# Performance work log

Measured on AMD Instinct MI355X. Metric: run time of the kernel, lower is better.

## Reference

```python
import jax, jax.numpy as jnp
import numpy as np

B, S, D = 4, 2048, 768
H = 12
HD = D // H  # 64


def setup_inputs() -> dict:
    key = jax.random.key(0)
    ks = jax.random.split(key, 7)
    scale = 1.0 / np.sqrt(D)
    return {
        "hidden_states": jax.random.normal(ks[0], (B, S, D), dtype=jnp.float32),
        "Wq": jax.random.normal(ks[1], (D, D), dtype=jnp.float32) * scale,
        "bq": jnp.zeros((D,), dtype=jnp.float32),
        "Wk": jax.random.normal(ks[2], (D, D), dtype=jnp.float32) * scale,
        "bk": jnp.zeros((D,), dtype=jnp.float32),
        "Wv": jax.random.normal(ks[3], (D, D), dtype=jnp.float32) * scale,
        "bv": jnp.zeros((D,), dtype=jnp.float32),
    }


def _split_heads(x):
    # [B, S, D] -> [B, H, S, HD]
    b, s, _ = x.shape
    return x.reshape(b, s, H, HD).transpose(0, 2, 1, 3)


def reference(hidden_states, Wq, bq, Wk, bk, Wv, bv):
    q = _split_heads(hidden_states @ Wq + bq)
    k = _split_heads(hidden_states @ Wk + bk)
    v = _split_heads(hidden_states @ Wv + bv)
    # [B, H, S, S] attention scores (naive full materialization, as in source)
    scores = jnp.einsum("bhqd,bhkd->bhqk", q, k) / jnp.sqrt(jnp.float32(HD))
    attn = jax.nn.softmax(scores, axis=-1)  # dropout = identity (eval)
    ctx = jnp.einsum("bhqk,bhkd->bhqd", attn, v)
    # [B, H, S, HD] -> [B, S, D]
    return ctx.transpose(0, 2, 1, 3).reshape(hidden_states.shape[0], -1, H * HD)
```

## Files before the change

### kernel.cpp

```cpp
#include <hip/hip_runtime.h>
#include <cmath>

#define B_  4
#define S_  2048
#define D_  768
#define H_  12
#define HD_ 64
#define BH_ 48
#define N3_ 2304
#define M_  8192

typedef _Float16 half8  __attribute__((ext_vector_type(8)));
typedef _Float16 half4v __attribute__((ext_vector_type(4)));
typedef __fp16   fp16x2 __attribute__((ext_vector_type(2)));
typedef __fp16   fp16x4 __attribute__((ext_vector_type(4)));
typedef float    floatx4 __attribute__((ext_vector_type(4)));

typedef const unsigned int __attribute__((address_space(1)))* gas_u32;
typedef unsigned int __attribute__((address_space(3)))* las_u32;

#define LOG2E 1.4426950408889634f
#define NEG_C (-5.0f * 1.4426950408889634f)

__global__ void cvt_f32_f16(const float* __restrict__ src,
                            _Float16* __restrict__ dst, int n) {
  int i = (blockIdx.x * blockDim.x + threadIdx.x) * 4;
  if (i < n) {
    float4 v = *(const float4*)(src + i);
    half4v h = {(_Float16)v.x, (_Float16)v.y, (_Float16)v.z, (_Float16)v.w};
    *(half4v*)(dst + i) = h;
  }
}

__global__ __launch_bounds__(256) void transpose_cvt_w(
    const float* __restrict__ W, _Float16* __restrict__ Wt) {
  __shared__ float tile[32][33];
  const int k0 = blockIdx.x * 32, n0 = blockIdx.y * 32;
  const int r = threadIdx.x >> 3, c4 = (threadIdx.x & 7) * 4;
  float4 v = *(const float4*)(W + (size_t)(k0 + r) * D_ + n0 + c4);
  tile[r][c4 + 0] = v.x; tile[r][c4 + 1] = v.y;
  tile[r][c4 + 2] = v.z; tile[r][c4 + 3] = v.w;
  __syncthreads();
  half4v h = {(_Float16)tile[c4 + 0][r], (_Float16)tile[c4 + 1][r],
              (_Float16)tile[c4 + 2][r], (_Float16)tile[c4 + 3][r]};
  *(half4v*)(Wt + (size_t)(n0 + r) * D_ + k0 + c4) = h;
}

__global__ __launch_bounds__(256, 3) void gemm_qkv(
    const _Float16* __restrict__ Xh, const _Float16* __restrict__ Wt3,
    const float* __restrict__ bq, const float* __restrict__ bk,
    const float* __restrict__ bv,
    _Float16* __restrict__ qo, _Float16* __restrict__ ko,
    _Float16* __restrict__ vto) {
  __shared__ __align__(16) char gsm[36864];
  _Float16* As = (_Float16*)gsm;
  _Float16* Bs = (_Float16*)(gsm + 16384);
  const int tid = threadIdx.x;
  const int w = tid >> 6, lane = tid & 63;
  const int tx = lane & 15, quad = lane >> 4;
  const int nBase = blockIdx.x * 128;
  const int mBase = blockIdx.y * 128;
  const int wm = (w & 1) * 64, wn = (w >> 1) * 64;

  floatx4 acc[4][4];
  #pragma unroll
  for (int i = 0; i < 4; ++i)
    #pragma unroll
    for (int j = 0; j < 4; ++j) acc[i][j] = (floatx4){0.f, 0.f, 0.f, 0.f};

  const int ldRow = lane >> 3;
  const int ldCol = (lane & 7) * 8;

  for (int k0 = 0; k0 < D_; k0 += 64) {
    __syncthreads();
    #pragma unroll
    for (int io = 0; io < 4; ++io) {
      int row = w * 32 + io * 8;
      const _Float16* ga =
          Xh + (size_t)(mBase + row + ldRow) * D_ + k0 + ldCol;
      __builtin_amdgcn_global_load_lds((gas_u32)(const void*)ga,
                                       (las_u32)(void*)&As[row * 64], 16, 0, 0);
      const _Float16* gb =
          Wt3 + (size_t)(nBase + row + ldRow) * D_ + k0 + ldCol;
      __builtin_amdgcn_global_load_lds((gas_u32)(const void*)gb,
                                       (las_u32)(void*)&Bs[row * 64], 16, 0, 0);
    }
    __syncthreads();

    half8 af0[4], af1[4], bf0[4], bf1[4];
    #pragma unroll
    for (int i = 0; i < 4; ++i) {
      af0[i] = *(const half8*)&As[(wm + 16 * i + tx) * 64 + quad * 8];
      af1[i] = *(const half8*)&As[(wm + 16 * i + tx) * 64 + quad * 8 + 32];
    }
    #pragma unroll
    for (int j = 0; j < 4; ++j) {
      bf0[j] = *(const half8*)&Bs[(wn + 16 * j + tx) * 64 + quad * 8];
      bf1[j] = *(const half8*)&Bs[(wn + 16 * j + tx) * 64 + quad * 8 + 32];
    }
    #pragma unroll
    for (int i = 0; i < 4; ++i)
      #pragma unroll
      for (int j = 0; j < 4; ++j) {
        acc[i][j] = __builtin_amdgcn_mfma_f32_16x16x32_f16(af0[i], bf0[j], acc[i][j], 0, 0, 0);
        acc[i][j] = __builtin_amdgcn_mfma_f32_16x16x32_f16(af1[i], bf1[j], acc[i][j], 0, 0, 0);
      }
  }

  const int region = nBase / 768;
  const int b = mBase >> 11;
  const int sBase = mBase & (S_ - 1);

  if (region < 2) {
    const float scale = (region == 0) ? 0.125f * LOG2E : 1.0f;
    const float* bias = (region == 0) ? bq : bk;
    _Float16* dst = (region == 0) ? qo : ko;
    const int nLoc = (nBase % 768) + wn;
    #pragma unroll
    for (int j = 0; j < 4; ++j) {
      int n = nLoc + 16 * j + tx;
      int h = n >> 6, d = n & 63;
      float bb = bias[n];
      #pragma unroll
      for (int i = 0; i < 4; ++i)
        #pragma unroll
        for (int r = 0; r < 4; ++r) {
          int m = mBase + wm + 16 * i + quad * 4 + r;
          int s = m & (S_ - 1);
          dst[((size_t)(b * H_ + h) * S_ + s) * HD_ + d] =
              (_Float16)((acc[i][j][r] + bb) * scale);
        }
    }
  } else {
    __syncthreads();
    _Float16 (*Ct)[144] = (_Float16(*)[144])gsm;
    const int nV = nBase - 1536;
    #pragma unroll
    for (int j = 0; j < 4; ++j) {
      int nl = wn + 16 * j + tx;
      float bb = bv[nV + nl];
      #pragma unroll
      for (int i = 0; i < 4; ++i)
        #pragma unroll
        for (int r = 0; r < 4; ++r)
          Ct[nl][wm + 16 * i + quad * 4 + r] = (_Float16)(acc[i][j][r] + bb);
    }
    __syncthreads();
    #pragma unroll
    for (int io = 0; io < 8; ++io) {
      int idx = io * 256 + tid;
      int nl = idx >> 4;
      int sc = (idx & 15) * 8;
      int n = nV + nl, h = n >> 6, d = n & 63;
      half8 hv = *(const half8*)&Ct[nl][sc];
      *(half8*)(vto + (((size_t)(b * H_ + h) * HD_) + d) * S_ + sBase + sc) = hv;
    }
  }
}

__global__ __launch_bounds__(512, 4) void attn_mfma(
    const _Float16* __restrict__ qh, const _Float16* __restrict__ kh,
    const _Float16* __restrict__ vth, float* __restrict__ out) {
  __shared__ __align__(16) char smem[36864];
  _Float16 (*Ks2)[64][72]  = (_Float16(*)[64][72])smem;
  _Float16 (*Vts2)[64][72] = (_Float16(*)[64][72])(smem + 18432);
  float (*Of)[68] = (float(*)[68])smem;
  float* lbuf = (float*)(smem + 34816);

  const int tid = threadIdx.x;
  const int bh = blockIdx.y;
  const int qBase = blockIdx.x * 128;
  const int w = tid >> 6, lane = tid & 63;
  const int half = w >> 2, wq = w & 3;
  const int tx = lane & 15, quad = lane >> 4;

  const _Float16* kp = kh + (size_t)bh * S_ * HD_;
  const _Float16* vtp = vth + (size_t)bh * HD_ * S_;

  half8 bq[2][2];
  #pragma unroll
  for (int g = 0; g < 2; ++g) {
    const _Float16* qp =
        qh + ((size_t)bh * S_ + qBase + wq * 32 + g * 16 + tx) * HD_;
    bq[g][0] = *(const half8*)(qp + quad * 8);
    bq[g][1] = *(const half8*)(qp + quad * 8 + 32);
  }

  floatx4 o_acc[2][4];
  #pragma unroll
  for (int g = 0; g < 2; ++g)
    #pragma unroll
    for (int j = 0; j < 4; ++j) o_acc[g][j] = (floatx4){0.f, 0.f, 0.f, 0.f};
  float l_loc[2] = {0.f, 0.f};

  const int th = tid & 255;
  const int kr = th >> 3, kc = (th & 7) * 8;

  for (int it = 0; it < S_ / 128; ++it) {
    const int kt0 = it * 128 + half * 64;
    __syncthreads();
    #pragma unroll
    for (int io = 0; io < 2; ++io) {
      int row = kr + io * 32;
      *(half8*)&Ks2[half][row][kc] =
          *(const half8*)(kp + (size_t)(kt0 + row) * HD_ + kc);
      *(half8*)&Vts2[half][row][kc] =
          *(const half8*)(vtp + (size_t)row * S_ + kt0 + kc);
    }
    __syncthreads();

    #pragma unroll
    for (int t = 0; t < 4; ++t) {
      half8 ka0 = *(const half8*)&Ks2[half][16 * t + tx][quad * 8];
      half8 ka1 = *(const half8*)&Ks2[half][16 * t + tx][quad * 8 + 32];
      fp16x4 pf[2];
      #pragma unroll
      for (int g = 0; g < 2; ++g) {
        __builtin_amdgcn_s_setprio(1);
        floatx4 st = __builtin_amdgcn_mfma_f32_16x16x32_f16(
            ka0, bq[g][0], (floatx4){NEG_C, NEG_C, NEG_C, NEG_C}, 0, 0, 0);
        st = __builtin_amdgcn_mfma_f32_16x16x32_f16(ka1, bq[g][1], st, 0, 0, 0);
        __builtin_amdgcn_s_setprio(0);
        float p0 = __builtin_amdgcn_exp2f(st[0]);
        float p1 = __builtin_amdgcn_exp2f(st[1]);
        float p2 = __builtin_amdgcn_exp2f(st[2]);
        float p3 = __builtin_amdgcn_exp2f(st[3]);
        l_loc[g] += (p0 + p1) + (p2 + p3);
        fp16x2 lo = __builtin_amdgcn_cvt_pkrtz(p0, p1);
        fp16x2 hi = __builtin_amdgcn_cvt_pkrtz(p2, p3);
        pf[g] = (fp16x4){lo.x, lo.y, hi.x, hi.y};
      }
      __builtin_amdgcn_s_setprio(1);
      #pragma unroll
      for (int j = 0; j < 4; ++j) {
        fp16x4 vb = *(const fp16x4*)&Vts2[half][16 * j + tx][16 * t + quad * 4];
        o_acc[0][j] = __builtin_amdgcn_mfma_f32_16x16x16f16(pf[0], vb, o_acc[0][j], 0, 0, 0);
        o_acc[1][j] = __builtin_amdgcn_mfma_f32_16x16x16f16(pf[1], vb, o_acc[1][j], 0, 0, 0);
      }
      __builtin_amdgcn_s_setprio(0);
    }
  }

  float lg[2];
  #pragma unroll
  for (int g = 0; g < 2; ++g) {
    lg[g] = l_loc[g];
    lg[g] += __shfl_xor(lg[g], 16, 64);
    lg[g] += __shfl_xor(lg[g], 32, 64);
  }

  __syncthreads();
  if (half == 1) {
    #pragma unroll
    for (int g = 0; g < 2; ++g) {
      int rowB = wq * 32 + g * 16;
      #pragma unroll
      for (int j = 0; j < 4; ++j)
        #pragma unroll
        for (int r = 0; r < 4; ++r)
          Of[rowB + quad * 4 + r][16 * j + tx] = o_acc[g][j][r];
      if (quad == 0) lbuf[rowB + tx] = lg[g];
    }
  }
  __syncthreads();
  if (half == 0) {
    const int b = bh / H_;
    const int h = bh % H_;
    #pragma unroll
    for (int g = 0; g < 2; ++g) {
      int rowB = wq * 32 + g * 16;
      float ltot = lg[g] + lbuf[rowB + tx];
      #pragma unroll
      for (int r = 0; r < 4; ++r) {
        int m = quad * 4 + r;
        float inv = 1.f / __shfl(ltot, m, 64);
        int s = qBase + rowB + m;
        #pragma unroll
        for (int j = 0; j < 4; ++j) {
          float o = o_acc[g][j][r] + Of[rowB + m][16 * j + tx];
          out[((size_t)b * S_ + s) * D_ + h * HD_ + 16 * j + tx] = o * inv;
        }
      }
    }
  }
}

extern "C" void kernel_launch(void* const* d_in, const int* in_sizes, int n_in,
                              void* d_out, int out_size, void* d_ws, size_t ws_size,
                              hipStream_t stream) {
  const float* X  = (const float*)d_in[0];
  const float* Wq = (const float*)d_in[1];
  const float* bq = (const float*)d_in[2];
  const float* Wk = (const float*)d_in[3];
  const float* bk = (const float*)d_in[4];
  const float* Wv = (const float*)d_in[5];
  const float* bv = (const float*)d_in[6];
  float* out = (float*)d_out;

  const size_t nX = (size_t)M_ * D_;
  const size_t nW = (size_t)D_ * D_;
  const size_t nQ = (size_t)BH_ * S_ * HD_;

  _Float16* Xh  = (_Float16*)d_ws;
  _Float16* Wt3 = Xh + nX;
  _Float16* qhb = Wt3 + 3 * nW;
  _Float16* khb = qhb + nQ;
  _Float16* vtb = khb + nQ;

  cvt_f32_f16<<<(int)(nX / 4 / 256), 256, 0, stream>>>(X, Xh, (int)nX);

  dim3 gridT(D_ / 32, D_ / 32);
  transpose_cvt_w<<<gridT, 256, 0, stream>>>(Wq, Wt3);
  transpose_cvt_w<<<gridT, 256, 0, stream>>>(Wk, Wt3 + nW);
  transpose_cvt_w<<<gridT, 256, 0, stream>>>(Wv, Wt3 + 2 * nW);

  dim3 gridG(N3_ / 128, M_ / 128);
  gemm_qkv<<<gridG, 256, 0, stream>>>(Xh, Wt3, bq, bk, bv, qhb, khb, vtb);

  dim3 gridA(S_ / 128, BH_);
  attn_mfma<<<gridA, 512, 0, stream>>>(qhb, khb, vtb, out);
}
```

Baseline: 210.7 us.

## Use 16x16x32 MFMA for PV with permuted K rows and register-prefetched tiles

Computes two QK^T score tiles per step and feeds the exponentiated probabilities as half8 operands into the K=32 MFMA for the PV product. This halves the number of PV MFMA instructions and V LDS reads. K rows are stored in LDS under a permutation so the score layout lines up with the wider MFMA's k-index order. The next K/V tile is also prefetched into registers during compute, so global loads overlap with MFMA work. This costs more registers, which could hurt occupancy under the 512x4 launch bounds.

```diff
diff --git a/kernel.cpp b/kernel.cpp
--- a/kernel.cpp
+++ b/kernel.cpp
@@ -173,6 +173,7 @@
   const int w = tid >> 6, lane = tid & 63;
   const int half = w >> 2, wq = w & 3;
   const int tx = lane & 15, quad = lane >> 4;
+  const int rbase = 16 * (tx >> 3) + 4 * ((tx >> 2) & 1) + (tx & 3);
 
   const _Float16* kp = kh + (size_t)bh * S_ * HD_;
   const _Float16* vtp = vth + (size_t)bh * HD_ * S_;
@@ -196,46 +197,82 @@
   const int th = tid & 255;
   const int kr = th >> 3, kc = (th & 7) * 8;
 
-  for (int it = 0; it < S_ / 128; ++it) {
-    const int kt0 = it * 128 + half * 64;
-    __syncthreads();
+  const int NT = S_ / 128;
+  half8 kst[2], vst[2];
+  {
+    const int kt0 = half * 64;
     #pragma unroll
     for (int io = 0; io < 2; ++io) {
       int row = kr + io * 32;
-      *(half8*)&Ks2[half][row][kc] =
-          *(const half8*)(kp + (size_t)(kt0 + row) * HD_ + kc);
-      *(half8*)&Vts2[half][row][kc] =
-          *(const half8*)(vtp + (size_t)row * S_ + kt0 + kc);
-    }
-    __syncthreads();
-
-    #pragma unroll
-    for (int t = 0; t < 4; ++t) {
-      half8 ka0 = *(const half8*)&Ks2[half][16 * t + tx][quad * 8];
-      half8 ka1 = *(const half8*)&Ks2[half][16 * t + tx][quad * 8 + 32];
-      fp16x4 pf[2];
+      kst[io] = *(const half8*)(kp + (size_t)(kt0 + row) * HD_ + kc);
+      vst[io] = *(const half8*)(vtp + (size_t)row * S_ + kt0 + kc);
+    }
+  }
+
+  for (int it = 0; it < NT; ++it) {
+    __syncthreads();
+    #pragma unroll
+    for (int io = 0; io < 2; ++io) {
+      int row = kr + io * 32;
+      int srow = (row & 51) | ((row & 4) << 1) | ((row & 8) >> 1);
+      *(half8*)&Ks2[half][srow][kc] = kst[io];
+      *(half8*)&Vts2[half][row][kc] = vst[io];
+    }
+    if (it + 1 < NT) {
+      const int kt1 = (it + 1) * 128 + half * 64;
+      #pragma unroll
+      for (int io = 0; io < 2; ++io) {
+        int row = kr + io * 32;
+        kst[io] = *(const half8*)(kp + (size_t)(kt1 + row) * HD_ + kc);
+        vst[io] = *(const half8*)(vtp + (size_t)row * S_ + kt1 + kc);
+      }
+    }
+    __syncthreads();
+
+    #pragma unroll
+    for (int T = 0; T < 2; ++T) {
+      floatx4 st[2][2];
+      #pragma unroll
+      for (int u = 0; u < 2; ++u) {
+        int lrow = rbase + 32 * T + 8 * u;
+        half8 ka0 = *(const half8*)&Ks2[half][lrow][quad * 8];
+        half8 ka1 = *(const half8*)&Ks2[half][lrow][quad * 8 + 32];
+        __builtin_amdgcn_s_setprio(1);
+        #pragma unroll
+        for (int g = 0; g < 2; ++g) {
+          st[g][u] = __builtin_amdgcn_mfma_f32_16x16x32_f16(
+              ka0, bq[g][0], (floatx4){NEG_C, NEG_C, NEG_C, NEG_C}, 0, 0, 0);
+          st[g][u] = __builtin_amdgcn_mfma_f32_16x16x32_f16(
+              ka1, bq[g][1], st[g][u], 0, 0, 0);
+        }
+        __builtin_amdgcn_s_setprio(0);
+      }
+      half8 pf[2];
       #pragma unroll
       for (int g = 0; g < 2; ++g) {
-        __builtin_amdgcn_s_setprio(1);
-        floatx4 st = __builtin_amdgcn_mfma_f32_16x16x32_f16(
-            ka0, bq[g][0], (floatx4){NEG_C, NEG_C, NEG_C, NEG_C}, 0, 0, 0);
-        st = __builtin_amdgcn_mfma_f32_16x16x32_f16(ka1, bq[g][1], st, 0, 0, 0);
-        __builtin_amdgcn_s_setprio(0);
-        float p0 = __builtin_amdgcn_exp2f(st[0]);
-        float p1 = __builtin_amdgcn_exp2f(st[1]);
-        float p2 = __builtin_amdgcn_exp2f(st[2]);
-        float p3 = __builtin_amdgcn_exp2f(st[3]);
-        l_loc[g] += (p0 + p1) + (p2 + p3);
-        fp16x2 lo = __builtin_amdgcn_cvt_pkrtz(p0, p1);
-        fp16x2 hi = __builtin_amdgcn_cvt_pkrtz(p2, p3);
-        pf[g] = (fp16x4){lo.x, lo.y, hi.x, hi.y};
+        float p0 = __builtin_amdgcn_exp2f(st[g][0][0]);
+        float p1 = __builtin_amdgcn_exp2f(st[g][0][1]);
+        float p2 = __builtin_amdgcn_exp2f(st[g][0][2]);
+        float p3 = __builtin_amdgcn_exp2f(st[g][0][3]);
+        float p4 = __builtin_amdgcn_exp2f(st[g][1][0]);
+        float p5 = __builtin_amdgcn_exp2f(st[g][1][1]);
+        float p6 = __builtin_amdgcn_exp2f(st[g][1][2]);
+        float p7 = __builtin_amdgcn_exp2f(st[g][1][3]);
+        l_loc[g] += ((p0 + p1) + (p2 + p3)) + ((p4 + p5) + (p6 + p7));
+        fp16x2 q0 = __builtin_amdgcn_cvt_pkrtz(p0, p1);
+        fp16x2 q1 = __builtin_amdgcn_cvt_pkrtz(p2, p3);
+        fp16x2 q2 = __builtin_amdgcn_cvt_pkrtz(p4, p5);
+        fp16x2 q3 = __builtin_amdgcn_cvt_pkrtz(p6, p7);
+        pf[g] = (half8){(_Float16)q0.x, (_Float16)q0.y, (_Float16)q1.x,
+                        (_Float16)q1.y, (_Float16)q2.x, (_Float16)q2.y,
+                        (_Float16)q3.x, (_Float16)q3.y};
       }
       __builtin_amdgcn_s_setprio(1);
       #pragma unroll
       for (int j = 0; j < 4; ++j) {
-        fp16x4 vb = *(const fp16x4*)&Vts2[half][16 * j + tx][16 * t + quad * 4];
-        o_acc[0][j] = __builtin_amdgcn_mfma_f32_16x16x16f16(pf[0], vb, o_acc[0][j], 0, 0, 0);
-        o_acc[1][j] = __builtin_amdgcn_mfma_f32_16x16x16f16(pf[1], vb, o_acc[1][j], 0, 0, 0);
+        half8 vb = *(const half8*)&Vts2[half][16 * j + tx][32 * T + quad * 8];
+        o_acc[0][j] = __builtin_amdgcn_mfma_f32_16x16x32_f16(pf[0], vb, o_acc[0][j], 0, 0, 0);
+        o_acc[1][j] = __builtin_amdgcn_mfma_f32_16x16x32_f16(pf[1], vb, o_acc[1][j], 0, 0, 0);
       }
       __builtin_amdgcn_s_setprio(0);
     }
```

Result: slower. 372.2 us (+76.7%).
